# Performance work log

Measured on AMD Instinct MI355X. Metric: run time of the kernel, lower is better.

Reference implementation:

```python
import jax, jax.numpy as jnp
import numpy as np

# alphas = cfg.model.mmd.alphas ** k for k in range(-3, 2), base = 2.0
ALPHAS = tuple(2.0 ** k for k in range(-3, 2))


def _sq_dist(x, y):
    # x: (..., n, c), y: (..., m, c) -> (..., n, m) squared euclidean distance
    xx = jnp.sum(x * x, axis=-1)[..., :, None]
    yy = jnp.sum(y * y, axis=-1)[..., None, :]
    xy = jnp.einsum('...ic,...jc->...ij', x, y)
    return jnp.maximum(xx + yy - 2.0 * xy, 0.0)


def _multi_gauss(d2):
    # sum over alphas of exp(-alpha * dist^2); d2 is already the squared distance
    return sum(jnp.exp(-a * d2) for a in ALPHAS)


def setup_inputs() -> dict:
    key = jax.random.key(0)
    k1, k2, k3, k4 = jax.random.split(key, 4)
    b, ns, nq, ng, nsf, nqf, c = 8, 5, 75, 4, 49, 49, 64
    support_xf = jax.random.normal(k1, (b, ns, ng, nsf, c), dtype=jnp.float32)
    query_xf = jax.random.normal(k2, (b, nq, ng, nqf, c), dtype=jnp.float32)
    beta = jax.random.uniform(k3, (b, nq, ns, ng, nsf), dtype=jnp.float32)
    gamma = jax.random.uniform(k4, (b, nq, ns, ng, nqf), dtype=jnp.float32)
    return {"support_xf": support_xf, "query_xf": query_xf, "beta": beta, "gamma": gamma}


def reference(support_xf, query_xf, beta, gamma):
    # support_xf: (b, ns, ng, nsf, c); query_xf: (b, nq, ng, nqf, c)
    # beta, gamma: (b, nq, ns, ng, nsf/nqf)
    Kss = _multi_gauss(_sq_dist(support_xf, support_xf))   # (b, ns, ng, nsf, nsf)
    Kqq = _multi_gauss(_sq_dist(query_xf, query_xf))       # (b, nq, ng, nqf, nqf)

    # cross squared distances: (b, nq, ns, ng, nsf, nqf)
    s_sq = jnp.sum(support_xf * support_xf, axis=-1)        # (b, ns, ng, nsf)
    q_sq = jnp.sum(query_xf * query_xf, axis=-1)            # (b, nq, ng, nqf)
    sq_dot = jnp.einsum('bsgic,bvgjc->bvsgij', support_xf, query_xf)
    d2_sq = jnp.maximum(
        s_sq[:, None, :, :, :, None] + q_sq[:, :, None, :, None, :] - 2.0 * sq_dot, 0.0)
    Ksq = _multi_gauss(d2_sq)                               # (b, nq, ns, ng, nsf, nqf)

    # beta^T Kss beta  (Kss broadcast over the query axis)
    mmd_s = jnp.einsum('bvsgi,bsgij,bvsgj->bvsg', beta, Kss, beta)
    # gamma^T Kqq gamma (Kqq broadcast over the support axis)
    mmd_q = jnp.einsum('bvsgi,bvgij,bvsgj->bvsg', gamma, Kqq, gamma)
    # beta^T Ksq gamma
    mmd_sq = jnp.einsum('bvsgi,bvsgij,bvsgj->bvsg', beta, Ksq, gamma)

    mmd_dis = mmd_s + mmd_q - 2.0 * mmd_sq                  # (b, nq, ns, ng)
    return jnp.mean(mmd_dis, axis=-1)                       # (b, nq, ns)
```

## Files before the change

### kernel.cpp

```cpp
#include <hip/hip_runtime.h>

#define BB 8
#define NS 5
#define NQ 75
#define NG 4
#define NF 49
#define CDIM 64

#define SUPROWS (BB * NG * NS * 64)
#define QRYROWS (BB * NQ * NG * 64)
#define TOTROWS (SUPROWS + QRYROWS)
#define NOUT (BB * NQ * NS)
#define NCROSS (BB * NQ * NG * 2)
#define NFORM (BB * NG * NS)

typedef __attribute__((ext_vector_type(8))) short bf16x8;
typedef __attribute__((ext_vector_type(16))) float f32x16;

__device__ __forceinline__ float multi_gauss(float d2) {
    d2 = fmaxf(d2, 0.f);
    float e  = __expf(-0.125f * d2);
    float e2 = e * e, e4 = e2 * e2, e8 = e4 * e4, e16 = e8 * e8;
    return e + e2 + e4 + e8 + e16;
}

__device__ __forceinline__ float multi_gauss2(float arg) {
    float e  = __builtin_amdgcn_exp2f(fminf(arg, 0.f));
    float e2 = e * e, e4 = e2 * e2, e8 = e4 * e4, e16 = e8 * e8;
    return ((e + e2) + (e4 + e8)) + e16;
}

__device__ __forceinline__ unsigned short f2bf(float x) {
    union { float f; unsigned u; } c; c.f = x;
    unsigned r = c.u + 0x7FFFu + ((c.u >> 16) & 1u);
    return (unsigned short)(r >> 16);
}
__device__ __forceinline__ float bf2f(unsigned short h) {
    union { float f; unsigned u; } c; c.u = ((unsigned)h) << 16; return c.f;
}

__device__ __forceinline__ float wred(float x) {
    for (int o = 32; o; o >>= 1) x += __shfl_down(x, o, 64);
    return x;
}

__global__ __launch_bounds__(256) void prep(
    const float* __restrict__ sup, const float* __restrict__ qry,
    unsigned short* __restrict__ whi, float* __restrict__ wssq,
    float* __restrict__ out)
{
    int u = blockIdx.x * 256 + threadIdx.x;
    if (u < NOUT) out[u] = 0.f;

    int row = u >> 4;
    int c = (u & 15) * 4;

    const float* src = nullptr;
    if (row < SUPROWS) {
        int i = row & 63, t6 = row >> 6;
        int s = t6 % NS, bg = t6 / NS;
        int g = bg & 3, b = bg >> 2;
        if (i < NF) src = sup + ((size_t)(((b * NS + s) * NG + g) * NF + i)) * CDIM + c;
    } else {
        int r2 = row - SUPROWS;
        int j = r2 & 63, t6 = r2 >> 6;
        int g = t6 & 3, v = (t6 >> 2) % NQ, b = t6 / (NQ * NG);
        if (j < NF) src = qry + ((size_t)(((b * NQ + v) * NG + g) * NF + j)) * CDIM + c;
    }
    float4 x = make_float4(0.f, 0.f, 0.f, 0.f);
    if (src) x = *(const float4*)src;
    ushort4 h4;
    h4.x = f2bf(x.x); h4.y = f2bf(x.y); h4.z = f2bf(x.z); h4.w = f2bf(x.w);
    ((ushort4*)whi)[u] = h4;

    float v2 = x.x * x.x + x.y * x.y + x.z * x.z + x.w * x.w;
    v2 += __shfl_down(v2, 8, 64);
    v2 += __shfl_down(v2, 4, 64);
    v2 += __shfl_down(v2, 2, 64);
    v2 += __shfl_down(v2, 1, 64);
    if ((u & 15) == 0) wssq[row] = v2;
}

__global__ __launch_bounds__(256, 5) void mmd_main(
    const unsigned short* __restrict__ whi, const float* __restrict__ wssq,
    const float* __restrict__ beta, const float* __restrict__ gamma,
    float* __restrict__ out)
{
    __shared__ __align__(16) union {
        struct {
            float sbeta[NS][64], sgam[NS][64];
            float ssq[384];
            float red_sq[NS], red_qq[NS];
        } c;
        struct {
            unsigned short Kt[64][72];
            unsigned short Bt[96][72];
            float red_s[96];
        } f;
    } sm;

    int blk = blockIdx.x;
    int t = threadIdx.x;
    int w = t >> 6, lane = t & 63, lrow = lane & 31, lhalf = lane >> 5;
    const bf16x8* W = (const bf16x8*)whi;

    if (blk < NCROSS) {
        int h = blk & 1;
        int g = (blk >> 1) & 3;
        int v = (blk >> 3) % NQ;
        int b = blk / (NQ * NG * 2);
        int qc = h * 32;

        int srow0 = (b * NG + g) * (NS * 64);
        int qrow0 = SUPROWS + ((b * NQ + v) * NG + g) * 64;

        for (int u = t; u < 384; u += 256)
            sm.c.ssq[u] = (u < 320) ? wssq[srow0 + u] : wssq[qrow0 + (u - 320)];
        for (int u = t; u < NS * 64; u += 256) {
            int s = u >> 6, i = u & 63;
            float bvv = 0.f, gvv = 0.f;
            if (i < NF) {
                size_t base = (size_t)(((b * NQ + v) * NS + s) * NG + g) * NF + i;
                bvv = beta[base]; gvv = gamma[base];
            }
            sm.c.sbeta[s][i] = bvv; sm.c.sgam[s][i] = gvv;
        }
        if (t < NS) { sm.c.red_sq[t] = 0.f; sm.c.red_qq[t] = 0.f; }

        f32x16 acc[3];
#pragma unroll
        for (int mi = 0; mi < 3; ++mi)
#pragma unroll
            for (int q = 0; q < 16; ++q) acc[mi][q] = 0.f;

        int a2row = (w < 2) ? (srow0 + (8 + w) * 32 + lrow)
                            : (qrow0 + (w - 2) * 32 + lrow);
#pragma unroll
        for (int kc = 0; kc < 4; ++kc) {
            int ko = kc * 2 + lhalf;
            bf16x8 bh = W[(qrow0 + qc + lrow) * 8 + ko];
            bf16x8 a0 = W[(srow0 + w * 32 + lrow) * 8 + ko];
            bf16x8 a1 = W[(srow0 + (w + 4) * 32 + lrow) * 8 + ko];
            bf16x8 a2 = W[a2row * 8 + ko];
            acc[0] = __builtin_amdgcn_mfma_f32_32x32x16_bf16(a0, bh, acc[0], 0, 0, 0);
            acc[1] = __builtin_amdgcn_mfma_f32_32x32x16_bf16(a1, bh, acc[1], 0, 0, 0);
            acc[2] = __builtin_amdgcn_mfma_f32_32x32x16_bf16(a2, bh, acc[2], 0, 0, 0);
        }
        __syncthreads();

        const float c2  = -0.18033688f;
        const float k2c =  0.36067376f;
        float qsq = sm.c.ssq[320 + qc + lrow];
        float c2q = c2 * qsq;

#pragma unroll
        for (int mi = 0; mi < 3; ++mi) {
            int mt = (mi < 2) ? (w + 4 * mi) : ((w < 2) ? (8 + w) : -1);
            if (mt >= 0) {
                int s = mt >> 1;
                int ioff = (mt & 1) * 32;
                float tsum = 0.f;
#pragma unroll
                for (int grp = 0; grp < 4; ++grp) {
                    int rbase = grp * 8 + 4 * lhalf;
                    float4 sqv = *(const float4*)&sm.c.ssq[mt * 32 + rbase];
                    float4 bvv = *(const float4*)&sm.c.sbeta[s][ioff + rbase];
#pragma unroll
                    for (int q = 0; q < 4; ++q) {
                        float sq = (q == 0) ? sqv.x : (q == 1) ? sqv.y : (q == 2) ? sqv.z : sqv.w;
                        float bv = (q == 0) ? bvv.x : (q == 1) ? bvv.y : (q == 2) ? bvv.z : bvv.w;
                        float arg = fmaf(k2c, acc[mi][grp * 4 + q], fmaf(c2, sq, c2q));
                        tsum = fmaf(bv, multi_gauss2(arg), tsum);
                    }
                }
                tsum *= sm.c.sgam[s][qc + lrow];
                tsum = wred(tsum);
                if (lane == 0) atomicAdd(&sm.c.red_sq[s], tsum);
            } else {
                int qoff = (w - 2) * 32;
                float qs[NS] = {0.f, 0.f, 0.f, 0.f, 0.f};
#pragma unroll
                for (int grp = 0; grp < 4; ++grp) {
                    int rbase = grp * 8 + 4 * lhalf;
                    float4 sqv = *(const float4*)&sm.c.ssq[320 + qoff + rbase];
                    float kvv[4];
#pragma unroll
                    for (int q = 0; q < 4; ++q) {
                        float sq = (q == 0) ? sqv.x : (q == 1) ? sqv.y : (q == 2) ? sqv.z : sqv.w;
                        int row = qoff + rbase + q;
                        float arg = fmaf(k2c, acc[mi][grp * 4 + q], fmaf(c2, sq, c2q));
                        kvv[q] = (row == qc + lrow) ? 5.0f : multi_gauss2(arg);
                    }
#pragma unroll
                    for (int s = 0; s < NS; ++s) {
                        float4 gi = *(const float4*)&sm.c.sgam[s][qoff + rbase];
                        qs[s] = fmaf(gi.x, kvv[0], qs[s]);
                        qs[s] = fmaf(gi.y, kvv[1], qs[s]);
                        qs[s] = fmaf(gi.z, kvv[2], qs[s]);
                        qs[s] = fmaf(gi.w, kvv[3], qs[s]);
                    }
                }
#pragma unroll
                for (int s = 0; s < NS; ++s) {
                    float r = wred(qs[s] * sm.c.sgam[s][qc + lrow]);
                    if (lane == 0) atomicAdd(&sm.c.red_qq[s], r);
                }
            }
        }
        __syncthreads();
        if (t < NS)
            atomicAdd(&out[((size_t)b * NQ + v) * NS + t],
                      0.25f * (sm.c.red_qq[t] - 2.f * sm.c.red_sq[t]));
    } else {
        int k = blk - NCROSS;
        int s = k % NS;
        int bg = k / NS;
        int g = bg & 3, b = bg >> 2;
        int row0 = (b * NG + g) * (NS * 64) + s * 64;

        for (int u = t; u < 96 * 64; u += 256) {
            int v = u >> 6, j = u & 63;
            unsigned short val = 0;
            if (v < NQ && j < NF)
                val = f2bf(beta[(size_t)(((b * NQ + v) * NS + s) * NG + g) * NF + j]);
            sm.f.Bt[v][j] = val;
        }
        if (t < 96) sm.f.red_s[t] = 0.f;

        int mt = w >> 1, nt = w & 1;
        f32x16 acc;
#pragma unroll
        for (int q = 0; q < 16; ++q) acc[q] = 0.f;
#pragma unroll
        for (int kc = 0; kc < 4; ++kc) {
            int ko = kc * 2 + lhalf;
            bf16x8 a  = W[(row0 + mt * 32 + lrow) * 8 + ko];
            bf16x8 bf = W[(row0 + nt * 32 + lrow) * 8 + ko];
            acc = __builtin_amdgcn_mfma_f32_32x32x16_bf16(a, bf, acc, 0, 0, 0);
        }
        int cj = nt * 32 + lrow;
        float sqj = wssq[row0 + cj];
#pragma unroll
        for (int reg = 0; reg < 16; ++reg) {
            int ri = mt * 32 + (reg & 3) + 8 * (reg >> 2) + 4 * lhalf;
            float kv = (ri == cj) ? 5.0f
                     : multi_gauss(wssq[row0 + ri] + sqj - 2.f * acc[reg]);
            sm.f.Kt[ri][cj] = f2bf(kv);
        }
        __syncthreads();

#pragma unroll
        for (int pass = 0; pass < 2; ++pass) {
            int T = (pass == 0) ? w : ((w < 2) ? 4 + w : -1);
            if (T < 0) continue;
            int mt2 = T / 3, nt2 = T % 3;
            f32x16 yacc;
#pragma unroll
            for (int q = 0; q < 16; ++q) yacc[q] = 0.f;
#pragma unroll
            for (int kc = 0; kc < 4; ++kc) {
                int koff = kc * 16 + lhalf * 8;
                bf16x8 af = *(const bf16x8*)&sm.f.Kt[mt2 * 32 + lrow][koff];
                bf16x8 bf = *(const bf16x8*)&sm.f.Bt[nt2 * 32 + lrow][koff];
                yacc = __builtin_amdgcn_mfma_f32_32x32x16_bf16(af, bf, yacc, 0, 0, 0);
            }
            int v = nt2 * 32 + lrow;
            float p = 0.f;
#pragma unroll
            for (int reg = 0; reg < 16; ++reg) {
                int i = mt2 * 32 + (reg & 3) + 8 * (reg >> 2) + 4 * lhalf;
                p = fmaf(yacc[reg], bf2f(sm.f.Bt[v][i]), p);
            }
            p += __shfl_xor(p, 32, 64);
            if (lane < 32) atomicAdd(&sm.f.red_s[v], p);
        }
        __syncthreads();
        if (t < NQ)
            atomicAdd(&out[((size_t)b * NQ + t) * NS + s], 0.25f * sm.f.red_s[t]);
    }
}

extern "C" void kernel_launch(void* const* d_in, const int* in_sizes, int n_in,
                              void* d_out, int out_size, void* d_ws, size_t ws_size,
                              hipStream_t stream) {
    const float* sup   = (const float*)d_in[0];
    const float* qry   = (const float*)d_in[1];
    const float* beta  = (const float*)d_in[2];
    const float* gamma = (const float*)d_in[3];
    float* out = (float*)d_out;

    unsigned short* whi = (unsigned short*)d_ws;
    float* wssq = (float*)(whi + (size_t)TOTROWS * 64);

    prep<<<(TOTROWS * 16) / 256, 256, 0, stream>>>(sup, qry, whi, wssq, out);
    mmd_main<<<NCROSS + NFORM, 256, 0, stream>>>(whi, wssq, beta, gamma, out);
}
```

Before: 132.9 us.

## Pack support rows densely, move Kss quadratic form into prep, split Kqq blocks

Support features are now packed densely, 245 rows per (b,g) padded to 256 instead of 5×64. The cross blocks therefore need two MFMA tiles per wave instead of three, and they split partial sums across support-set boundaries. The beta^T Kss beta computation moves into the prep kernel as 40 blocks that loop over groups and write the output directly, replacing the separate zero-initialisation. The Kqq term moves into its own block type, so cross blocks no longer carry the extra query-query tile. This cuts wasted padded MFMA work and register pressure (launch bounds raised to 6). It also makes the output correctness depend on the prep kernel writing before the main kernel's atomic adds, which stream ordering guarantees.

```diff
diff --git a/kernel.cpp b/kernel.cpp
--- a/kernel.cpp
+++ b/kernel.cpp
@@ -7,12 +7,13 @@
 #define NF 49
 #define CDIM 64
 
-#define SUPROWS (BB * NG * NS * 64)
-#define QRYROWS (BB * NQ * NG * 64)
-#define TOTROWS (SUPROWS + QRYROWS)
-#define NOUT (BB * NQ * NS)
+#define SUP2 8192
+#define QB   8192
+#define QRYR (BB * NQ * NG * 64)
+#define TOT2 (SUP2 + QRYR)
+#define NFORM (BB * NS)
 #define NCROSS (BB * NQ * NG * 2)
-#define NFORM (BB * NG * NS)
+#define NQQ (BB * NQ * NG)
 
 typedef __attribute__((ext_vector_type(8))) short bf16x8;
 typedef __attribute__((ext_vector_type(16))) float f32x16;
@@ -23,13 +24,11 @@
     float e2 = e * e, e4 = e2 * e2, e8 = e4 * e4, e16 = e8 * e8;
     return e + e2 + e4 + e8 + e16;
 }
-
 __device__ __forceinline__ float multi_gauss2(float arg) {
     float e  = __builtin_amdgcn_exp2f(fminf(arg, 0.f));
     float e2 = e * e, e4 = e2 * e2, e8 = e4 * e4, e16 = e8 * e8;
     return ((e + e2) + (e4 + e8)) + e16;
 }
-
 __device__ __forceinline__ unsigned short f2bf(float x) {
     union { float f; unsigned u; } c; c.f = x;
     unsigned r = c.u + 0x7FFFu + ((c.u >> 16) & 1u);
@@ -38,7 +37,6 @@
 __device__ __forceinline__ float bf2f(unsigned short h) {
     union { float f; unsigned u; } c; c.u = ((unsigned)h) << 16; return c.f;
 }
-
 __device__ __forceinline__ float wred(float x) {
     for (int o = 32; o; o >>= 1) x += __shfl_down(x, o, 64);
     return x;
@@ -46,63 +44,147 @@
 
 __global__ __launch_bounds__(256) void prep(
     const float* __restrict__ sup, const float* __restrict__ qry,
+    const float* __restrict__ beta,
     unsigned short* __restrict__ whi, float* __restrict__ wssq,
     float* __restrict__ out)
 {
-    int u = blockIdx.x * 256 + threadIdx.x;
-    if (u < NOUT) out[u] = 0.f;
-
-    int row = u >> 4;
-    int c = (u & 15) * 4;
-
-    const float* src = nullptr;
-    if (row < SUPROWS) {
-        int i = row & 63, t6 = row >> 6;
-        int s = t6 % NS, bg = t6 / NS;
-        int g = bg & 3, b = bg >> 2;
-        if (i < NF) src = sup + ((size_t)(((b * NS + s) * NG + g) * NF + i)) * CDIM + c;
-    } else {
-        int r2 = row - SUPROWS;
-        int j = r2 & 63, t6 = r2 >> 6;
-        int g = t6 & 3, v = (t6 >> 2) % NQ, b = t6 / (NQ * NG);
-        if (j < NF) src = qry + ((size_t)(((b * NQ + v) * NG + g) * NF + j)) * CDIM + c;
+    __shared__ __align__(16) unsigned short A[64 * 72];
+    __shared__ __align__(16) unsigned short Bt[96 * 72];
+    __shared__ float fssq[64];
+    __shared__ float red_s[96];
+
+    int blk = blockIdx.x;
+    int t = threadIdx.x;
+    int w = t >> 6, lane = t & 63, lrow = lane & 31, lhalf = lane >> 5;
+
+    if (blk >= NFORM) {
+        int idx = (blk - NFORM) * 256 + t;
+        int row = idx >> 4, c4 = idx & 15;
+        const float* src = nullptr;
+        if (row < SUP2) {
+            int bg = row >> 8, p = row & 255;
+            int b = bg >> 2, g = bg & 3;
+            int s = p / 49, i = p - s * 49;
+            if (p < 245) src = sup + ((size_t)(((b * NS + s) * NG + g) * NF + i)) * CDIM + c4 * 4;
+        } else {
+            int r2 = row - SUP2;
+            int t6 = r2 >> 6, j = r2 & 63;
+            int g = t6 & 3, v = (t6 >> 2) % NQ, b = t6 / (NQ * NG);
+            if (j < NF) src = qry + ((size_t)(((b * NQ + v) * NG + g) * NF + j)) * CDIM + c4 * 4;
+        }
+        float4 x = make_float4(0.f, 0.f, 0.f, 0.f);
+        if (src) x = *(const float4*)src;
+        ushort4 h4;
+        h4.x = f2bf(x.x); h4.y = f2bf(x.y); h4.z = f2bf(x.z); h4.w = f2bf(x.w);
+        ((ushort4*)whi)[idx] = h4;
+        float v2 = x.x * x.x + x.y * x.y + x.z * x.z + x.w * x.w;
+        v2 += __shfl_down(v2, 8, 64);
+        v2 += __shfl_down(v2, 4, 64);
+        v2 += __shfl_down(v2, 2, 64);
+        v2 += __shfl_down(v2, 1, 64);
+        if ((idx & 15) == 0) wssq[row] = v2;
+        return;
     }
-    float4 x = make_float4(0.f, 0.f, 0.f, 0.f);
-    if (src) x = *(const float4*)src;
-    ushort4 h4;
-    h4.x = f2bf(x.x); h4.y = f2bf(x.y); h4.z = f2bf(x.z); h4.w = f2bf(x.w);
-    ((ushort4*)whi)[u] = h4;
-
-    float v2 = x.x * x.x + x.y * x.y + x.z * x.z + x.w * x.w;
-    v2 += __shfl_down(v2, 8, 64);
-    v2 += __shfl_down(v2, 4, 64);
-    v2 += __shfl_down(v2, 2, 64);
-    v2 += __shfl_down(v2, 1, 64);
-    if ((u & 15) == 0) wssq[row] = v2;
-}
-
-__global__ __launch_bounds__(256, 5) void mmd_main(
+
+    int b = blk / NS, s = blk % NS;
+    if (t < 96) red_s[t] = 0.f;
+
+    for (int g = 0; g < NG; ++g) {
+        __syncthreads();
+        for (int u = t; u < 1024; u += 256) {
+            int i = u >> 4, c4 = u & 15;
+            float4 x = make_float4(0.f, 0.f, 0.f, 0.f);
+            if (i < NF)
+                x = *(const float4*)(sup + ((size_t)(((b * NS + s) * NG + g) * NF + i)) * CDIM + c4 * 4);
+            ushort4 h4;
+            h4.x = f2bf(x.x); h4.y = f2bf(x.y); h4.z = f2bf(x.z); h4.w = f2bf(x.w);
+            *(ushort4*)&A[i * 72 + c4 * 4] = h4;
+            float v2 = x.x * x.x + x.y * x.y + x.z * x.z + x.w * x.w;
+            v2 += __shfl_down(v2, 8, 64);
+            v2 += __shfl_down(v2, 4, 64);
+            v2 += __shfl_down(v2, 2, 64);
+            v2 += __shfl_down(v2, 1, 64);
+            if ((u & 15) == 0) fssq[i] = v2;
+        }
+        for (int u = t; u < 96 * 64; u += 256) {
+            int v = u >> 6, j = u & 63;
+            unsigned short val = 0;
+            if (v < NQ && j < NF)
+                val = f2bf(beta[(size_t)(((b * NQ + v) * NS + s) * NG + g) * NF + j]);
+            Bt[v * 72 + j] = val;
+        }
+        __syncthreads();
+
+        int mt = w >> 1, nt = w & 1;
+        f32x16 acc;
+#pragma unroll
+        for (int q = 0; q < 16; ++q) acc[q] = 0.f;
+#pragma unroll
+        for (int kc = 0; kc < 4; ++kc) {
+            int ko = kc * 2 + lhalf;
+            bf16x8 a  = *(const bf16x8*)&A[(mt * 32 + lrow) * 72 + ko * 8];
+            bf16x8 bb = *(const bf16x8*)&A[(nt * 32 + lrow) * 72 + ko * 8];
+            acc = __builtin_amdgcn_mfma_f32_32x32x16_bf16(a, bb, acc, 0, 0, 0);
+        }
+        __syncthreads();
+
+        int cj = nt * 32 + lrow;
+        float sqj = fssq[cj];
+#pragma unroll
+        for (int reg = 0; reg < 16; ++reg) {
+            int ri = mt * 32 + (reg & 3) + 8 * (reg >> 2) + 4 * lhalf;
+            float kv = (ri == cj) ? 5.0f : multi_gauss(fssq[ri] + sqj - 2.f * acc[reg]);
+            A[ri * 72 + cj] = f2bf(kv);
+        }
+        __syncthreads();
+
+#pragma unroll
+        for (int pass = 0; pass < 2; ++pass) {
+            int T = (pass == 0) ? w : ((w < 2) ? 4 + w : -1);
+            if (T < 0) continue;
+            int m = T & 1, n = T >> 1;
+            f32x16 yacc;
+#pragma unroll
+            for (int q = 0; q < 16; ++q) yacc[q] = 0.f;
+#pragma unroll
+            for (int kc = 0; kc < 4; ++kc) {
+                int ko = kc * 2 + lhalf;
+                bf16x8 af = *(const bf16x8*)&A[(m * 32 + lrow) * 72 + ko * 8];
+                bf16x8 bf = *(const bf16x8*)&Bt[(n * 32 + lrow) * 72 + ko * 8];
+                yacc = __builtin_amdgcn_mfma_f32_32x32x16_bf16(af, bf, yacc, 0, 0, 0);
+            }
+            int vcol = n * 32 + lrow;
+            float p = 0.f;
+#pragma unroll
+            for (int reg = 0; reg < 16; ++reg) {
+                int i = m * 32 + (reg & 3) + 8 * (reg >> 2) + 4 * lhalf;
+                p = fmaf(yacc[reg], bf2f(Bt[vcol * 72 + i]), p);
+            }
+            p += __shfl_xor(p, 32, 64);
+            if (lane < 32) atomicAdd(&red_s[vcol], p);
+        }
+    }
+    __syncthreads();
+    if (t < NQ)
+        out[((size_t)b * NQ + t) * NS + s] = 0.25f * red_s[t];
+}
+
+__global__ __launch_bounds__(256, 6) void mmd_main(
     const unsigned short* __restrict__ whi, const float* __restrict__ wssq,
     const float* __restrict__ beta, const float* __restrict__ gamma,
     float* __restrict__ out)
 {
     __shared__ __align__(16) union {
-        struct {
-            float sbeta[NS][64], sgam[NS][64];
-            float ssq[384];
-            float red_sq[NS], red_qq[NS];
-        } c;
-        struct {
-            unsigned short Kt[64][72];
-            unsigned short Bt[96][72];
-            float red_s[96];
-        } f;
+        struct { float ssqS[256]; float sbetaF[256]; float red_sq[NS]; } c;
+        struct { float sgam[NS][64]; float ssqQ[64]; float red_qq[NS]; } q;
     } sm;
 
     int blk = blockIdx.x;
     int t = threadIdx.x;
     int w = t >> 6, lane = t & 63, lrow = lane & 31, lhalf = lane >> 5;
     const bf16x8* W = (const bf16x8*)whi;
+    const float c2  = -0.18033688f;
+    const float k2c =  0.36067376f;
 
     if (blk < NCROSS) {
         int h = blk & 1;
@@ -111,172 +193,142 @@
         int b = blk / (NQ * NG * 2);
         int qc = h * 32;
 
-        int srow0 = (b * NG + g) * (NS * 64);
-        int qrow0 = SUPROWS + ((b * NQ + v) * NG + g) * 64;
-
-        for (int u = t; u < 384; u += 256)
-            sm.c.ssq[u] = (u < 320) ? wssq[srow0 + u] : wssq[qrow0 + (u - 320)];
+        int srow0 = (b * NG + g) * 256;
+        int qrow0 = QB + ((b * NQ + v) * NG + g) * 64;
+
+        {
+            int p = t;
+            sm.c.ssqS[p] = wssq[srow0 + p];
+            int s = p / 49, i = p - s * 49;
+            sm.c.sbetaF[p] = (p < 245)
+                ? beta[(size_t)(((b * NQ + v) * NS + s) * NG + g) * NF + i] : 0.f;
+            if (t < NS) sm.c.red_sq[t] = 0.f;
+        }
+        int qcol = qc + lrow;
+        float qsq = wssq[qrow0 + qcol];
+        float gamv[NS];
+#pragma unroll
+        for (int s = 0; s < NS; ++s)
+            gamv[s] = (qcol < NF)
+                ? gamma[(size_t)(((b * NQ + v) * NS + s) * NG + g) * NF + qcol] : 0.f;
+
+        f32x16 acc[2];
+#pragma unroll
+        for (int mi = 0; mi < 2; ++mi)
+#pragma unroll
+            for (int q = 0; q < 16; ++q) acc[mi][q] = 0.f;
+#pragma unroll
+        for (int kc = 0; kc < 4; ++kc) {
+            int ko = kc * 2 + lhalf;
+            bf16x8 bh = W[(qrow0 + qcol) * 8 + ko];
+            bf16x8 a0 = W[(srow0 + w * 32 + lrow) * 8 + ko];
+            bf16x8 a1 = W[(srow0 + (w + 4) * 32 + lrow) * 8 + ko];
+            acc[0] = __builtin_amdgcn_mfma_f32_32x32x16_bf16(a0, bh, acc[0], 0, 0, 0);
+            acc[1] = __builtin_amdgcn_mfma_f32_32x32x16_bf16(a1, bh, acc[1], 0, 0, 0);
+        }
+        __syncthreads();
+
+        float c2q = c2 * qsq;
+#pragma unroll
+        for (int mi = 0; mi < 2; ++mi) {
+            int mt = w + 4 * mi;
+            int s_lo = (mt * 32) / 49;
+            int bnd = (s_lo + 1) * 49;
+            int s_hi = (s_lo < 4) ? s_lo + 1 : 4;
+            float tA = 0.f, tB = 0.f;
+#pragma unroll
+            for (int grp = 0; grp < 4; ++grp) {
+                int rbase = mt * 32 + grp * 8 + 4 * lhalf;
+                float4 sqv = *(const float4*)&sm.c.ssqS[rbase];
+                float4 bvv = *(const float4*)&sm.c.sbetaF[rbase];
+#pragma unroll
+                for (int q = 0; q < 4; ++q) {
+                    float sq = (q == 0) ? sqv.x : (q == 1) ? sqv.y : (q == 2) ? sqv.z : sqv.w;
+                    float bv = (q == 0) ? bvv.x : (q == 1) ? bvv.y : (q == 2) ? bvv.z : bvv.w;
+                    float arg = fmaf(k2c, acc[mi][grp * 4 + q], fmaf(c2, sq, c2q));
+                    float con = bv * multi_gauss2(arg);
+                    bool lo = (rbase + q) < bnd;
+                    tA += lo ? con : 0.f;
+                    tB += lo ? 0.f : con;
+                }
+            }
+            tA *= gamv[s_lo];
+            tB *= gamv[s_hi];
+            tA = wred(tA);
+            tB = wred(tB);
+            if (lane == 0) {
+                atomicAdd(&sm.c.red_sq[s_lo], tA);
+                atomicAdd(&sm.c.red_sq[s_hi], tB);
+            }
+        }
+        __syncthreads();
+        if (t < NS)
+            atomicAdd(&out[((size_t)b * NQ + v) * NS + t], -0.5f * sm.c.red_sq[t]);
+    } else {
+        int k = blk - NCROSS;
+        int g = k & 3;
+        int v = (k >> 2) % NQ;
+        int b = k / (NQ * NG);
+        int qrow0 = QB + ((b * NQ + v) * NG + g) * 64;
+
         for (int u = t; u < NS * 64; u += 256) {
             int s = u >> 6, i = u & 63;
-            float bvv = 0.f, gvv = 0.f;
-            if (i < NF) {
-                size_t base = (size_t)(((b * NQ + v) * NS + s) * NG + g) * NF + i;
-                bvv = beta[base]; gvv = gamma[base];
-            }
-            sm.c.sbeta[s][i] = bvv; sm.c.sgam[s][i] = gvv;
-        }
-        if (t < NS) { sm.c.red_sq[t] = 0.f; sm.c.red_qq[t] = 0.f; }
-
-        f32x16 acc[3];
-#pragma unroll
-        for (int mi = 0; mi < 3; ++mi)
-#pragma unroll
-            for (int q = 0; q < 16; ++q) acc[mi][q] = 0.f;
-
-        int a2row = (w < 2) ? (srow0 + (8 + w) * 32 + lrow)
-                            : (qrow0 + (w - 2) * 32 + lrow);
+            sm.q.sgam[s][i] = (i < NF)
+                ? gamma[(size_t)(((b * NQ + v) * NS + s) * NG + g) * NF + i] : 0.f;
+        }
+        if (t < 64) sm.q.ssqQ[t] = wssq[qrow0 + t];
+        if (t < NS) sm.q.red_qq[t] = 0.f;
+
+        int mt = w >> 1, nt = w & 1;
+        f32x16 acc;
+#pragma unroll
+        for (int q = 0; q < 16; ++q) acc[q] = 0.f;
 #pragma unroll
         for (int kc = 0; kc < 4; ++kc) {
             int ko = kc * 2 + lhalf;
-            bf16x8 bh = W[(qrow0 + qc + lrow) * 8 + ko];
-            bf16x8 a0 = W[(srow0 + w * 32 + lrow) * 8 + ko];
-            bf16x8 a1 = W[(srow0 + (w + 4) * 32 + lrow) * 8 + ko];
-            bf16x8 a2 = W[a2row * 8 + ko];
-            acc[0] = __builtin_amdgcn_mfma_f32_32x32x16_bf16(a0, bh, acc[0], 0, 0, 0);
-            acc[1] = __builtin_amdgcn_mfma_f32_32x32x16_bf16(a1, bh, acc[1], 0, 0, 0);
-            acc[2] = __builtin_amdgcn_mfma_f32_32x32x16_bf16(a2, bh, acc[2], 0, 0, 0);
-        }
-        __syncthreads();
-
-        const float c2  = -0.18033688f;
-        const float k2c =  0.36067376f;
-        float qsq = sm.c.ssq[320 + qc + lrow];
-        float c2q = c2 * qsq;
-
-#pragma unroll
-        for (int mi = 0; mi < 3; ++mi) {
-            int mt = (mi < 2) ? (w + 4 * mi) : ((w < 2) ? (8 + w) : -1);
-            if (mt >= 0) {
-                int s = mt >> 1;
-                int ioff = (mt & 1) * 32;
-                float tsum = 0.f;
-#pragma unroll
-                for (int grp = 0; grp < 4; ++grp) {
-                    int rbase = grp * 8 + 4 * lhalf;
-                    float4 sqv = *(const float4*)&sm.c.ssq[mt * 32 + rbase];
-                    float4 bvv = *(const float4*)&sm.c.sbeta[s][ioff + rbase];
-#pragma unroll
-                    for (int q = 0; q < 4; ++q) {
-                        float sq = (q == 0) ? sqv.x : (q == 1) ? sqv.y : (q == 2) ? sqv.z : sqv.w;
-                        float bv = (q == 0) ? bvv.x : (q == 1) ? bvv.y : (q == 2) ? bvv.z : bvv.w;
-                        float arg = fmaf(k2c, acc[mi][grp * 4 + q], fmaf(c2, sq, c2q));
-                        tsum = fmaf(bv, multi_gauss2(arg), tsum);
-                    }
-                }
-                tsum *= sm.c.sgam[s][qc + lrow];
-                tsum = wred(tsum);
-                if (lane == 0) atomicAdd(&sm.c.red_sq[s], tsum);
-            } else {
-                int qoff = (w - 2) * 32;
-                float qs[NS] = {0.f, 0.f, 0.f, 0.f, 0.f};
-#pragma unroll
-                for (int grp = 0; grp < 4; ++grp) {
-                    int rbase = grp * 8 + 4 * lhalf;
-                    float4 sqv = *(const float4*)&sm.c.ssq[320 + qoff + rbase];
-                    float kvv[4];
-#pragma unroll
-                    for (int q = 0; q < 4; ++q) {
-                        float sq = (q == 0) ? sqv.x : (q == 1) ? sqv.y : (q == 2) ? sqv.z : sqv.w;
-                        int row = qoff + rbase + q;
-                        float arg = fmaf(k2c, acc[mi][grp * 4 + q], fmaf(c2, sq, c2q));
-                        kvv[q] = (row == qc + lrow) ? 5.0f : multi_gauss2(arg);
-                    }
-#pragma unroll
-                    for (int s = 0; s < NS; ++s) {
-                        float4 gi = *(const float4*)&sm.c.sgam[s][qoff + rbase];
-                        qs[s] = fmaf(gi.x, kvv[0], qs[s]);
-                        qs[s] = fmaf(gi.y, kvv[1], qs[s]);
-                        qs[s] = fmaf(gi.z, kvv[2], qs[s]);
-                        qs[s] = fmaf(gi.w, kvv[3], qs[s]);
-                    }
-                }
-#pragma unroll
-                for (int s = 0; s < NS; ++s) {
-                    float r = wred(qs[s] * sm.c.sgam[s][qc + lrow]);
-                    if (lane == 0) atomicAdd(&sm.c.red_qq[s], r);
-                }
-            }
+            bf16x8 a  = W[(qrow0 + mt * 32 + lrow) * 8 + ko];
+            bf16x8 bb = W[(qrow0 + nt * 32 + lrow) * 8 + ko];
+            acc = __builtin_amdgcn_mfma_f32_32x32x16_bf16(a, bb, acc, 0, 0, 0);
+        }
+        __syncthreads();
+
+        int col = nt * 32 + lrow;
+        float csq = sm.q.ssqQ[col];
+        float c2q = c2 * csq;
+        float gcol[NS];
+#pragma unroll
+        for (int s = 0; s < NS; ++s) gcol[s] = sm.q.sgam[s][col];
+
+        float qs[NS] = {0.f, 0.f, 0.f, 0.f, 0.f};
+#pragma unroll
+        for (int grp = 0; grp < 4; ++grp) {
+            int rbase = mt * 32 + grp * 8 + 4 * lhalf;
+            float4 sqv = *(const float4*)&sm.q.ssqQ[rbase];
+            float kvv[4];
+#pragma unroll
+            for (int q = 0; q < 4; ++q) {
+                float sq = (q == 0) ? sqv.x : (q == 1) ? sqv.y : (q == 2) ? sqv.z : sqv.w;
+                int row = rbase + q;
+                float arg = fmaf(k2c, acc[grp * 4 + q], fmaf(c2, sq, c2q));
+                kvv[q] = (row == col) ? 5.0f : multi_gauss2(arg);
+            }
+#pragma unroll
+            for (int s = 0; s < NS; ++s) {
+                float4 gi = *(const float4*)&sm.q.sgam[s][rbase];
+                qs[s] = fmaf(gi.x, kvv[0], qs[s]);
+                qs[s] = fmaf(gi.y, kvv[1], qs[s]);
+                qs[s] = fmaf(gi.z, kvv[2], qs[s]);
+                qs[s] = fmaf(gi.w, kvv[3], qs[s]);
+            }
+        }
+#pragma unroll
+        for (int s = 0; s < NS; ++s) {
+            float r = wred(qs[s] * gcol[s]);
+            if (lane == 0) atomicAdd(&sm.q.red_qq[s], r);
         }
         __syncthreads();
         if (t < NS)
-            atomicAdd(&out[((size_t)b * NQ + v) * NS + t],
-                      0.25f * (sm.c.red_qq[t] - 2.f * sm.c.red_sq[t]));
-    } else {
-        int k = blk - NCROSS;
-        int s = k % NS;
-        int bg = k / NS;
-        int g = bg & 3, b = bg >> 2;
-        int row0 = (b * NG + g) * (NS * 64) + s * 64;
-
-        for (int u = t; u < 96 * 64; u += 256) {
-            int v = u >> 6, j = u & 63;
-            unsigned short val = 0;
-            if (v < NQ && j < NF)
-                val = f2bf(beta[(size_t)(((b * NQ + v) * NS + s) * NG + g) * NF + j]);
-            sm.f.Bt[v][j] = val;
-        }
-        if (t < 96) sm.f.red_s[t] = 0.f;
-
-        int mt = w >> 1, nt = w & 1;
-        f32x16 acc;
-#pragma unroll
-        for (int q = 0; q < 16; ++q) acc[q] = 0.f;
-#pragma unroll
-        for (int kc = 0; kc < 4; ++kc) {
-            int ko = kc * 2 + lhalf;
-            bf16x8 a  = W[(row0 + mt * 32 + lrow) * 8 + ko];
-            bf16x8 bf = W[(row0 + nt * 32 + lrow) * 8 + ko];
-            acc = __builtin_amdgcn_mfma_f32_32x32x16_bf16(a, bf, acc, 0, 0, 0);
-        }
-        int cj = nt * 32 + lrow;
-        float sqj = wssq[row0 + cj];
-#pragma unroll
-        for (int reg = 0; reg < 16; ++reg) {
-            int ri = mt * 32 + (reg & 3) + 8 * (reg >> 2) + 4 * lhalf;
-            float kv = (ri == cj) ? 5.0f
-                     : multi_gauss(wssq[row0 + ri] + sqj - 2.f * acc[reg]);
-            sm.f.Kt[ri][cj] = f2bf(kv);
-        }
-        __syncthreads();
-
-#pragma unroll
-        for (int pass = 0; pass < 2; ++pass) {
-            int T = (pass == 0) ? w : ((w < 2) ? 4 + w : -1);
-            if (T < 0) continue;
-            int mt2 = T / 3, nt2 = T % 3;
-            f32x16 yacc;
-#pragma unroll
-            for (int q = 0; q < 16; ++q) yacc[q] = 0.f;
-#pragma unroll
-            for (int kc = 0; kc < 4; ++kc) {
-                int koff = kc * 16 + lhalf * 8;
-                bf16x8 af = *(const bf16x8*)&sm.f.Kt[mt2 * 32 + lrow][koff];
-                bf16x8 bf = *(const bf16x8*)&sm.f.Bt[nt2 * 32 + lrow][koff];
-                yacc = __builtin_amdgcn_mfma_f32_32x32x16_bf16(af, bf, yacc, 0, 0, 0);
-            }
-            int v = nt2 * 32 + lrow;
-            float p = 0.f;
-#pragma unroll
-            for (int reg = 0; reg < 16; ++reg) {
-                int i = mt2 * 32 + (reg & 3) + 8 * (reg >> 2) + 4 * lhalf;
-                p = fmaf(yacc[reg], bf2f(sm.f.Bt[v][i]), p);
-            }
-            p += __shfl_xor(p, 32, 64);
-            if (lane < 32) atomicAdd(&sm.f.red_s[v], p);
-        }
-        __syncthreads();
-        if (t < NQ)
-            atomicAdd(&out[((size_t)b * NQ + t) * NS + s], 0.25f * sm.f.red_s[t]);
+            atomicAdd(&out[((size_t)b * NQ + v) * NS + t], 0.25f * sm.q.red_qq[t]);
     }
 }
 
@@ -290,8 +342,8 @@
     float* out = (float*)d_out;
 
     unsigned short* whi = (unsigned short*)d_ws;
-    float* wssq = (float*)(whi + (size_t)TOTROWS * 64);
-
-    prep<<<(TOTROWS * 16) / 256, 256, 0, stream>>>(sup, qry, whi, wssq, out);
-    mmd_main<<<NCROSS + NFORM, 256, 0, stream>>>(whi, wssq, beta, gamma, out);
-}
+    float* wssq = (float*)(whi + (size_t)TOT2 * 64);
+
+    prep<<<NFORM + (TOT2 * 16) / 256, 256, 0, stream>>>(sup, qry, beta, whi, wssq, out);
+    mmd_main<<<NCROSS + NQQ, 256, 0, stream>>>(whi, wssq, beta, gamma, out);
+}
```

Result: slower. 180.0 us (+35.4%).
